# Optimization experiments

Hardware: AMD Instinct MI355X
Metric: run time of the kernel (lower is better)

The kernel has to match this reference:

```python
import jax, jax.numpy as jnp
import numpy as np

D = 256      # d_v
FF = 512     # ff_dim = max(hidden, d_v)
H = 4        # num_heads
K = 8        # max_set_size
L = 64       # subset universe length
NC = 32768   # n_chains
NB = 4096    # n_batch
EPS = 1e-8   # module eps for masked-mean denom


def setup_inputs() -> dict:
    key = jax.random.key(0)
    ks = jax.random.split(key, 24)
    s = 0.02
    mask = jax.random.randint(ks[2], (NC, L), 0, 2).astype(bool)
    inp = {
        "v": jax.random.normal(ks[0], (NB, L, D), jnp.float32),
        "batch_idx": jax.random.randint(ks[1], (NC,), 0, NB),
        "mask": mask,
        "count": mask.sum(axis=1).astype(jnp.float32),
        "pos_embed": jnp.zeros((1, K, D), jnp.float32),
        "ln1_w": jnp.ones((D,), jnp.float32),
        "ln1_b": jnp.zeros((D,), jnp.float32),
        "in_proj_w": jax.random.normal(ks[3], (3 * D, D), jnp.float32) * s,
        "in_proj_b": jnp.zeros((3 * D,), jnp.float32),
        "out_proj_w": jax.random.normal(ks[4], (D, D), jnp.float32) * s,
        "out_proj_b": jnp.zeros((D,), jnp.float32),
        "ln2_w": jnp.ones((D,), jnp.float32),
        "ln2_b": jnp.zeros((D,), jnp.float32),
        "ff1_w": jax.random.normal(ks[5], (FF, D), jnp.float32) * s,
        "ff1_b": jnp.zeros((FF,), jnp.float32),
        "ff2_w": jax.random.normal(ks[6], (D, FF), jnp.float32) * s,
        "ff2_b": jnp.zeros((D,), jnp.float32),
        "o1_w": jax.random.normal(ks[7], (FF, D + 1), jnp.float32) * s,
        "o1_b": jnp.zeros((FF,), jnp.float32),
        "o2_w": jax.random.normal(ks[8], (D, FF), jnp.float32) * s,
        "o2_b": jnp.zeros((D,), jnp.float32),
    }
    return inp


def _layernorm(x, w, b, eps=1e-5):
    mu = x.mean(-1, keepdims=True)
    var = ((x - mu) ** 2).mean(-1, keepdims=True)
    return (x - mu) * jax.lax.rsqrt(var + eps) * w + b


def reference(v, batch_idx, mask, count, pos_embed, ln1_w, ln1_b, in_proj_w,
              in_proj_b, out_proj_w, out_proj_b, ln2_w, ln2_b, ff1_w, ff1_b,
              ff2_w, ff2_b, o1_w, o1_b, o2_w, o2_b):
    nc, Lm = mask.shape
    # --- topk subset select (index-order packing) ---
    pos = jnp.arange(Lm, dtype=jnp.float32)
    scores = mask.astype(jnp.float32) * (float(Lm) - pos)[None, :]
    top_scores, top_idx = jax.lax.top_k(scores, K)
    picked0 = top_scores > 0
    sortable = jnp.where(picked0, top_idx, Lm)
    sortable = jnp.sort(sortable, axis=1)
    picked = sortable < Lm                       # [NC,K]
    safe_idx = jnp.where(picked, sortable, 0)
    # fused gather: chain_v[c, i] = v[batch_idx[c], i]
    packed = v[batch_idx[:, None], safe_idx]     # [NC,K,D]
    packed = packed * picked[..., None].astype(packed.dtype)
    x = packed + pos_embed[:, :K, :]
    # key padding mask; un-mask position 0 for fully-empty sets
    kpm = ~picked
    empty = jnp.all(kpm, axis=1)
    kpm = kpm.at[:, 0].set(jnp.where(empty, False, kpm[:, 0]))
    # --- one pre-norm transformer encoder layer ---
    h = _layernorm(x, ln1_w, ln1_b)
    qkv = h @ in_proj_w.T + in_proj_b
    q, k_, vv = jnp.split(qkv, 3, axis=-1)
    hd = D // H
    def heads(t):
        return t.reshape(nc, K, H, hd).transpose(0, 2, 1, 3)
    q, k_, vv = heads(q), heads(k_), heads(vv)
    att = jnp.einsum('bhqd,bhkd->bhqk', q, k_) / jnp.sqrt(jnp.float32(hd))
    att = jnp.where(kpm[:, None, None, :], -jnp.inf, att)
    att = jax.nn.softmax(att, axis=-1)
    ao = jnp.einsum('bhqk,bhkd->bhqd', att, vv).transpose(0, 2, 1, 3).reshape(nc, K, D)
    x = x + ao @ out_proj_w.T + out_proj_b
    h2 = _layernorm(x, ln2_w, ln2_b)
    x = x + jax.nn.gelu(h2 @ ff1_w.T + ff1_b, approximate=False) @ ff2_w.T + ff2_b
    # --- masked mean pool ---
    pf = picked.astype(x.dtype)
    denom = jnp.maximum(pf.sum(axis=1, keepdims=True), EPS)
    pooled = (x * pf[..., None]).sum(axis=1) / denom
    pooled = jnp.where(picked.any(axis=1, keepdims=True), pooled, jnp.zeros_like(pooled))
    # --- concat log(1+|S|) and project ---
    feat = jnp.concatenate([pooled, jnp.log1p(count)[:, None]], axis=-1)
    return jax.nn.gelu(feat @ o1_w.T + o1_b, approximate=False) @ o2_w.T + o2_b
```

## Files before the change

### kernel.cpp

```cpp
#include <hip/hip_runtime.h>
#include <hip/hip_bf16.h>
#include <math.h>

typedef short short8 __attribute__((ext_vector_type(8)));
typedef short short4v __attribute__((ext_vector_type(4)));
typedef float f32x4 __attribute__((ext_vector_type(4)));

#define NCC  32768
#define G    4

#define G1_OFF 0
#define G2_OFF 196608
#define G3_OFF 262144
#define G4_OFF 393216
#define O1_OFF 524288
#define O2_OFF 655360
#define SWZ_SHORTS 786432
#define W256_BYTE_OFF (SWZ_SHORTS * 2)
#define FLAG_BYTE_OFF (W256_BYTE_OFF + 2048)

#define PX2_ST 260
#define PGF_ST 520

__device__ __forceinline__ float gelu_f(float x) {
    return x * 0.5f * (1.0f + erff(x * 0.70710678118654752f));
}
__device__ __forceinline__ unsigned short f2bf(float f) {
    __hip_bfloat16 h = __float2bfloat16(f);
    return *reinterpret_cast<unsigned short*>(&h);
}
__device__ __forceinline__ int aswz(int row, int scol) {
    return row * 256 + (scol ^ ((row & 7) << 3));
}
__device__ __forceinline__ int qswz(int row, int scol) {
    return row * 512 + (scol ^ ((row & 7) << 3));
}
__device__ __forceinline__ int vtswz(int d, int j) {
    return d * 32 + (j ^ ((d & 7) << 2));
}

template<int KTS>
__device__ __forceinline__ void load_bgrp(short8 (&b)[KTS], const unsigned short* __restrict__ base) {
    #pragma unroll
    for (int kt = 0; kt < KTS; kt++)
        b[kt] = *reinterpret_cast<const short8*>(base + (size_t)kt * 512);
}

__global__ void conv_weights(const float* __restrict__ w1, const float* __restrict__ w2,
                             const float* __restrict__ w3, const float* __restrict__ w4,
                             const float* __restrict__ o1, const float* __restrict__ o2,
                             unsigned short* __restrict__ dst, float* __restrict__ w256) {
    int i = blockIdx.x * 256 + threadIdx.x;
    if (i < 98304) {
        const float* src; int kts, sk, base;
        if (i < 24576)      { src = w1; kts = 8;  sk = 256; base = 0; }
        else if (i < 32768) { src = w2; kts = 8;  sk = 256; base = 24576; }
        else if (i < 49152) { src = w3; kts = 8;  sk = 256; base = 32768; }
        else if (i < 65536) { src = w4; kts = 16; sk = 512; base = 49152; }
        else if (i < 81920) { src = o1; kts = 8;  sk = 257; base = 65536; }
        else                { src = o2; kts = 16; sk = 512; base = 81920; }
        int li   = i - base;
        int lane = li & 63;
        int fi   = li >> 6;
        int kt   = fi % kts;
        int nt   = fi / kts;
        int col  = nt * 16 + (lane & 15);
        int k    = kt * 32 + (lane >> 4) * 8;
        const float* s = src + (size_t)col * sk + k;
        unsigned short* d = dst + (size_t)i * 8;
        #pragma unroll
        for (int e = 0; e < 8; e++) d[e] = f2bf(s[e]);
    } else if (i < 98816) {
        int c = i - 98304;
        w256[c] = o1[(size_t)c * 257 + 256];
    }
}

__global__ void detect_mask_fmt(const unsigned int* __restrict__ mw, int nwords, int* __restrict__ flag) {
    __shared__ int s_bad_int, s_bad_float;
    if (threadIdx.x == 0) { s_bad_int = 0; s_bad_float = 0; }
    __syncthreads();
    int bad_int = 0, bad_float = 0;
    for (int i = threadIdx.x; i < nwords; i += blockDim.x) {
        unsigned int w = mw[i];
        if (w > 1u) bad_int = 1;
        if (w != 0u && w != 0x3F800000u) bad_float = 1;
    }
    if (bad_int)   atomicOr(&s_bad_int, 1);
    if (bad_float) atomicOr(&s_bad_float, 1);
    __syncthreads();
    if (threadIdx.x == 0)
        *flag = (!s_bad_int) ? 0 : ((!s_bad_float) ? 2 : 1);
}

__global__ __launch_bounds__(256, 2)
void tsa_main(const float* __restrict__ v,
              const int* __restrict__ batch_idx,
              const void* __restrict__ mask,
              const float* __restrict__ pos_embed,
              const float* __restrict__ ln1_w, const float* __restrict__ ln1_b,
              const float* __restrict__ in_proj_b,
              const float* __restrict__ out_proj_b,
              const float* __restrict__ ln2_w, const float* __restrict__ ln2_b,
              const float* __restrict__ ff1_b, const float* __restrict__ ff2_b,
              const unsigned short* __restrict__ wb,
              const int* __restrict__ mask_flag,
              float* __restrict__ out)
{
    __shared__ unsigned short qkbuf[32 * 512];
    __shared__ unsigned short abuf[32 * 256];
    __shared__ unsigned short attw_s[2][4][16][16];
    __shared__ int s_idx[G][8];
    __shared__ int s_m[G];
    __shared__ int s_bi[G];

    float* lnred = reinterpret_cast<float*>(qkbuf);
    float* px2   = reinterpret_cast<float*>(qkbuf + 2048);
    float* pgff  = reinterpret_cast<float*>(qkbuf + 8192);

    const int tid  = threadIdx.x;
    const int lane = tid & 63;
    const int wid  = tid >> 6;
    const int cq   = lane >> 4;
    const int cc   = lane & 15;
    const int cg0  = blockIdx.x * G;
    const int pair = wid >> 1;

    f32x4 xr[2][4];

    {
        int mf = *mask_flag;
        size_t base = (size_t)(cg0 + wid) * 64 + lane;
        int bit;
        if (mf == 0)      bit = ((const int*)mask)[base] != 0;
        else if (mf == 2) bit = ((const float*)mask)[base] != 0.0f;
        else              bit = ((const unsigned char*)mask)[base] != 0;
        unsigned long long bal = __ballot(bit);
        if (lane == 0) {
            int mm = 0; unsigned long long b = bal;
            while (b && mm < 8) { s_idx[wid][mm++] = __ffsll(b) - 1; b &= (b - 1); }
            for (int t = mm; t < 8; t++) s_idx[wid][t] = 0;
            s_m[wid]  = mm;
            s_bi[wid] = batch_idx[cg0 + wid];
        }
    }
    __syncthreads();

    auto do_gather = [&]() {
        #pragma unroll
        for (int mt = 0; mt < 2; mt++) {
            int c  = 2 * mt + (cq >> 1);
            int m  = s_m[c];
            int bi = s_bi[c];
            #pragma unroll
            for (int rr = 0; rr < 4; rr++) {
                int rowin = (cq & 1) * 4 + rr;
                int vidx  = s_idx[c][rowin];
                #pragma unroll
                for (int nt = 0; nt < 4; nt++) {
                    int col  = wid * 64 + nt * 16 + cc;
                    float pe = pos_embed[rowin * 256 + col];
                    float val = (rowin < m) ? v[((size_t)bi * 64 + vidx) * 256 + col] : 0.0f;
                    xr[mt][nt][rr] = val + pe;
                }
            }
        }
    };

    auto do_ln = [&](const float* __restrict__ lw, const float* __restrict__ lb) {
        float sm[2][4], sq[2][4];
        #pragma unroll
        for (int mt = 0; mt < 2; mt++)
            #pragma unroll
            for (int rr = 0; rr < 4; rr++) {
                float s = 0.f, q = 0.f;
                #pragma unroll
                for (int nt = 0; nt < 4; nt++) {
                    float x = xr[mt][nt][rr];
                    s += x; q += x * x;
                }
                sm[mt][rr] = s; sq[mt][rr] = q;
            }
        #pragma unroll
        for (int off = 1; off < 16; off <<= 1) {
            #pragma unroll
            for (int mt = 0; mt < 2; mt++)
                #pragma unroll
                for (int rr = 0; rr < 4; rr++) {
                    sm[mt][rr] += __shfl_xor(sm[mt][rr], off);
                    sq[mt][rr] += __shfl_xor(sq[mt][rr], off);
                }
        }
        if (cc == 0) {
            #pragma unroll
            for (int mt = 0; mt < 2; mt++)
                #pragma unroll
                for (int rr = 0; rr < 4; rr++) {
                    int row = mt * 16 + cq * 4 + rr;
                    lnred[(wid * 32 + row) * 2 + 0] = sm[mt][rr];
                    lnred[(wid * 32 + row) * 2 + 1] = sq[mt][rr];
                }
        }
        __syncthreads();
        float mu[2][4], rs[2][4];
        #pragma unroll
        for (int mt = 0; mt < 2; mt++)
            #pragma unroll
            for (int rr = 0; rr < 4; rr++) {
                int row = mt * 16 + cq * 4 + rr;
                float S = 0.f, Q = 0.f;
                #pragma unroll
                for (int w = 0; w < 4; w++) {
                    S += lnred[(w * 32 + row) * 2 + 0];
                    Q += lnred[(w * 32 + row) * 2 + 1];
                }
                float m_ = S * (1.0f / 256.0f);
                mu[mt][rr] = m_;
                rs[mt][rr] = rsqrtf(Q * (1.0f / 256.0f) - m_ * m_ + 1e-5f);
            }
        #pragma unroll
        for (int nt = 0; nt < 4; nt++) {
            int col = wid * 64 + nt * 16 + cc;
            float w_ = lw[col], b_ = lb[col];
            #pragma unroll
            for (int mt = 0; mt < 2; mt++)
                #pragma unroll
                for (int rr = 0; rr < 4; rr++) {
                    int row = mt * 16 + cq * 4 + rr;
                    abuf[aswz(row, col)] = f2bf((xr[mt][nt][rr] - mu[mt][rr]) * rs[mt][rr] * w_ + b_);
                }
        }
        __syncthreads();
    };

    auto load_a_abuf = [&](short8 (&a0)[8], short8 (&a1)[8]) {
        #pragma unroll
        for (int kt = 0; kt < 8; kt++) {
            a0[kt] = *reinterpret_cast<const short8*>(&abuf[aswz(cc,      kt * 32 + cq * 8)]);
            a1[kt] = *reinterpret_cast<const short8*>(&abuf[aswz(16 + cc, kt * 32 + cq * 8)]);
        }
    };

    do_gather();
    do_ln(ln1_w, ln1_b);

    {
        short8 a0[8], a1[8];
        load_a_abuf(a0, a1);
        __syncthreads();

        auto gbase = [&](int g) {
            int nt = g >> 1, kh = g & 1;
            int gnt = (nt < 8) ? (wid * 8 + nt) : (32 + wid * 4 + (nt - 8));
            return wb + G1_OFF + ((size_t)gnt * 8 + kh * 4) * 512 + lane * 8;
        };
        short8 bb[2][4];
        load_bgrp<4>(bb[0], gbase(0));
        f32x4 c0, c1;
        #pragma unroll
        for (int nt = 0; nt < 12; nt++) {
            #pragma unroll
            for (int kh = 0; kh < 2; kh++) {
                int g = nt * 2 + kh;
                if (g + 1 < 24) load_bgrp<4>(bb[(g + 1) & 1], gbase(g + 1));
                if (kh == 0) {
                    float b = (nt < 8) ? in_proj_b[wid * 128 + nt * 16 + cc]
                                       : in_proj_b[512 + wid * 64 + (nt - 8) * 16 + cc];
                    c0 = (f32x4){b, b, b, b};
                    c1 = (f32x4){b, b, b, b};
                }
                __builtin_amdgcn_s_setprio(1);
                #pragma unroll
                for (int kt = 0; kt < 4; kt++) {
                    c0 = __builtin_amdgcn_mfma_f32_16x16x32_bf16(a0[kh * 4 + kt], bb[g & 1][kt], c0, 0, 0, 0);
                    c1 = __builtin_amdgcn_mfma_f32_16x16x32_bf16(a1[kh * 4 + kt], bb[g & 1][kt], c1, 0, 0, 0);
                }
                __builtin_amdgcn_s_setprio(0);
            }
            if (nt < 8) {
                int col = wid * 128 + nt * 16 + cc;
                #pragma unroll
                for (int r = 0; r < 4; r++) {
                    qkbuf[qswz(cq * 4 + r, col)]      = f2bf(c0[r]);
                    qkbuf[qswz(16 + cq * 4 + r, col)] = f2bf(c1[r]);
                }
            } else {
                int d = wid * 64 + (nt - 8) * 16 + cc;
                short4v p0, p1;
                #pragma unroll
                for (int r = 0; r < 4; r++) { p0[r] = (short)f2bf(c0[r]); p1[r] = (short)f2bf(c1[r]); }
                *reinterpret_cast<short4v*>(&abuf[vtswz(d, cq * 4)])      = p0;
                *reinterpret_cast<short4v*>(&abuf[vtswz(d, 16 + cq * 4)]) = p1;
            }
        }
    }
    __syncthreads();

    do_gather();

    {
        #pragma unroll
        for (int hj = 0; hj < 2; hj++) {
            int h = (wid & 1) * 2 + hj;
            f32x4 c = {0.f, 0.f, 0.f, 0.f};
            #pragma unroll
            for (int kt = 0; kt < 2; kt++) {
                short8 qa = *reinterpret_cast<const short8*>(&qkbuf[qswz(pair * 16 + cc, h * 64 + cq * 8 + kt * 32)]);
                short8 kb = *reinterpret_cast<const short8*>(&qkbuf[qswz(pair * 16 + cc, 256 + h * 64 + cq * 8 + kt * 32)]);
                c = __builtin_amdgcn_mfma_f32_16x16x32_bf16(qa, kb, c, 0, 0, 0);
            }
            int jhalf = cc >> 3, jloc = cc & 7;
            #pragma unroll
            for (int r = 0; r < 4; r++) {
                int q = cq * 4 + r;
                int qhalf = q >> 3;
                int m = s_m[pair * 2 + qhalf];
                bool valid = (jhalf == qhalf) && (jloc < m);
                float s = valid ? c[r] * 0.125f : -1e30f;
                float mx = s;
                mx = fmaxf(mx, __shfl_xor(mx, 1));
                mx = fmaxf(mx, __shfl_xor(mx, 2));
                mx = fmaxf(mx, __shfl_xor(mx, 4));
                float e = valid ? __expf(s - mx) : 0.f;
                float se = e;
                se += __shfl_xor(se, 1);
                se += __shfl_xor(se, 2);
                se += __shfl_xor(se, 4);
                attw_s[pair][h][q][cc] = f2bf((se > 0.f) ? e / se : 0.f);
            }
        }
    }
    __syncthreads();

    {
        int jbg = pair * 16 + (cq & 1) * 8;
        #pragma unroll
        for (int hj = 0; hj < 2; hj++) {
            int h = (wid & 1) * 2 + hj;
            short8 pa;
            if (cq < 2) pa = *reinterpret_cast<const short8*>(&attw_s[pair][h][cc][cq * 8]);
            else        pa = (short8)((short)0);
            #pragma unroll
            for (int t = 0; t < 4; t++) {
                int d = h * 64 + t * 16 + cc;
                short4v lo = *reinterpret_cast<const short4v*>(&abuf[vtswz(d, jbg)]);
                short4v hi = *reinterpret_cast<const short4v*>(&abuf[vtswz(d, jbg + 4)]);
                union { short8 vv; short4v half2[2]; } u;
                u.half2[0] = lo; u.half2[1] = hi;
                f32x4 c = {0.f, 0.f, 0.f, 0.f};
                c = __builtin_amdgcn_mfma_f32_16x16x32_bf16(pa, u.vv, c, 0, 0, 0);
                #pragma unroll
                for (int r = 0; r < 4; r++)
                    qkbuf[qswz(pair * 16 + cq * 4 + r, d)] = f2bf(c[r]);
            }
        }
    }
    __syncthreads();

    {
        #pragma unroll
        for (int nt = 0; nt < 4; nt++) {
            float b = out_proj_b[wid * 64 + nt * 16 + cc];
            #pragma unroll
            for (int r = 0; r < 4; r++) { xr[0][nt][r] += b; xr[1][nt][r] += b; }
        }
        auto gbase = [&](int g) {
            int kh = g >> 2, nt = g & 3;
            return wb + G2_OFF + ((size_t)(wid * 4 + nt) * 8 + kh * 4) * 512 + lane * 8;
        };
        short8 bb[2][4];
        load_bgrp<4>(bb[0], gbase(0));
        #pragma unroll
        for (int kh = 0; kh < 2; kh++) {
            short8 a0h[4], a1h[4];
            #pragma unroll
            for (int kt = 0; kt < 4; kt++) {
                a0h[kt] = *reinterpret_cast<const short8*>(&qkbuf[qswz(cc,      kh * 128 + kt * 32 + cq * 8)]);
                a1h[kt] = *reinterpret_cast<const short8*>(&qkbuf[qswz(16 + cc, kh * 128 + kt * 32 + cq * 8)]);
            }
            #pragma unroll
            for (int nt = 0; nt < 4; nt++) {
                int g = kh * 4 + nt;
                if (g + 1 < 8) load_bgrp<4>(bb[(g + 1) & 1], gbase(g + 1));
                __builtin_amdgcn_s_setprio(1);
                #pragma unroll
                for (int kt = 0; kt < 4; kt++) {
                    xr[0][nt] = __builtin_amdgcn_mfma_f32_16x16x32_bf16(a0h[kt], bb[g & 1][kt], xr[0][nt], 0, 0, 0);
                    xr[1][nt] = __builtin_amdgcn_mfma_f32_16x16x32_bf16(a1h[kt], bb[g & 1][kt], xr[1][nt], 0, 0, 0);
                }
                __builtin_amdgcn_s_setprio(0);
            }
        }
    }
    __syncthreads();

    #pragma unroll
    for (int mt = 0; mt < 2; mt++) {
        int c = 2 * mt + (cq >> 1);
        int m = s_m[c];
        #pragma unroll
        for (int nt = 0; nt < 4; nt++) {
            float p = 0.f;
            #pragma unroll
            for (int rr = 0; rr < 4; rr++)
                if ((cq & 1) * 4 + rr < m) p += xr[mt][nt][rr];
            p += __shfl_xor(p, 16);
            if ((cq & 1) == 0) {
                int col = wid * 64 + nt * 16 + cc;
                px2[c * PX2_ST + col] = p;
            }
        }
    }

    do_ln(ln2_w, ln2_b);

    {
        short8 a0[8], a1[8];
        load_a_abuf(a0, a1);
        auto gbase = [&](int g) {
            int nt = g >> 1, kh = g & 1;
            return wb + G3_OFF + ((size_t)(wid * 8 + nt) * 8 + kh * 4) * 512 + lane * 8;
        };
        short8 bb[2][4];
        load_bgrp<4>(bb[0], gbase(0));
        f32x4 c0, c1;
        #pragma unroll
        for (int nt = 0; nt < 8; nt++) {
            #pragma unroll
            for (int kh = 0; kh < 2; kh++) {
                int g = nt * 2 + kh;
                if (g + 1 < 16) load_bgrp<4>(bb[(g + 1) & 1], gbase(g + 1));
                if (kh == 0) {
                    float b = ff1_b[wid * 128 + nt * 16 + cc];
                    c0 = (f32x4){b, b, b, b};
                    c1 = (f32x4){b, b, b, b};
                }
                __builtin_amdgcn_s_setprio(1);
                #pragma unroll
                for (int kt = 0; kt < 4; kt++) {
                    c0 = __builtin_amdgcn_mfma_f32_16x16x32_bf16(a0[kh * 4 + kt], bb[g & 1][kt], c0, 0, 0, 0);
                    c1 = __builtin_amdgcn_mfma_f32_16x16x32_bf16(a1[kh * 4 + kt], bb[g & 1][kt], c1, 0, 0, 0);
                }
                __builtin_amdgcn_s_setprio(0);
            }
            int col = wid * 128 + nt * 16 + cc;
            float s0 = 0.f, s1 = 0.f;
            int m0 = s_m[cq >> 1];
            int m1 = s_m[2 + (cq >> 1)];
            #pragma unroll
            for (int r = 0; r < 4; r++) {
                float g0 = gelu_f(c0[r]);
                float g1 = gelu_f(c1[r]);
                if ((cq & 1) * 4 + r < m0) s0 += g0;
                if ((cq & 1) * 4 + r < m1) s1 += g1;
            }
            s0 += __shfl_xor(s0, 16);
            s1 += __shfl_xor(s1, 16);
            if ((cq & 1) == 0) {
                pgff[(cq >> 1) * PGF_ST + col]       = s0;
                pgff[(2 + (cq >> 1)) * PGF_ST + col] = s1;
            }
        }
    }
    __syncthreads();

    {
        auto gbase = [&](int g) {
            int kh = g >> 2, nt = g & 3;
            return wb + G4_OFF + ((size_t)(wid * 4 + nt) * 16 + kh * 4) * 512 + lane * 8;
        };
        short8 bb[2][4];
        load_bgrp<4>(bb[0], gbase(0));
        f32x4 acc[4];
        #pragma unroll
        for (int nt = 0; nt < 4; nt++) acc[nt] = (f32x4){0.f, 0.f, 0.f, 0.f};
        #pragma unroll
        for (int kh = 0; kh < 4; kh++) {
            short8 af[4];
            #pragma unroll
            for (int kt = 0; kt < 4; kt++) {
                short8 t = (short8)((short)0);
                if (cc < 4) {
                    const float4* s4 = reinterpret_cast<const float4*>(&pgff[cc * PGF_ST + (kh * 4 + kt) * 32 + cq * 8]);
                    float4 x0 = s4[0];
                    float4 x1 = s4[1];
                    t[0] = (short)f2bf(x0.x); t[1] = (short)f2bf(x0.y);
                    t[2] = (short)f2bf(x0.z); t[3] = (short)f2bf(x0.w);
                    t[4] = (short)f2bf(x1.x); t[5] = (short)f2bf(x1.y);
                    t[6] = (short)f2bf(x1.z); t[7] = (short)f2bf(x1.w);
                }
                af[kt] = t;
            }
            #pragma unroll
            for (int nt = 0; nt < 4; nt++) {
                int g = kh * 4 + nt;
                if (g + 1 < 16) load_bgrp<4>(bb[(g + 1) & 1], gbase(g + 1));
                __builtin_amdgcn_s_setprio(1);
                #pragma unroll
                for (int kt = 0; kt < 4; kt++)
                    acc[nt] = __builtin_amdgcn_mfma_f32_16x16x32_bf16(af[kt], bb[g & 1][kt], acc[nt], 0, 0, 0);
                __builtin_amdgcn_s_setprio(0);
            }
        }
        if (cq == 0) {
            #pragma unroll
            for (int nt = 0; nt < 4; nt++) {
                int col = wid * 64 + nt * 16 + cc;
                float b4 = ff2_b[col];
                #pragma unroll
                for (int r = 0; r < 4; r++) {
                    int m = s_m[r];
                    float val = 0.f;
                    if (m > 0) val = (px2[r * PX2_ST + col] + acc[nt][r]) / (float)m + b4;
                    out[(size_t)(cg0 + r) * 256 + col] = val;
                }
            }
        }
    }
}

__global__ __launch_bounds__(256, 2)
void tsa_head(const float* __restrict__ count,
              const float* __restrict__ o1_b, const float* __restrict__ o2_b,
              const unsigned short* __restrict__ wb, const float* __restrict__ w256,
              float* __restrict__ out)
{
    __shared__ unsigned short fbuf[32 * 256];
    __shared__ unsigned short gbuf[32 * 512];
    __shared__ float cbuf[32];

    const int tid  = threadIdx.x;
    const int lane = tid & 63;
    const int wid  = tid >> 6;
    const int cq   = lane >> 4;
    const int cc   = lane & 15;
    const int c0b  = blockIdx.x * 32;

    for (int i = tid; i < 32 * 256; i += 256) {
        int row = i >> 8, col = i & 255;
        fbuf[aswz(row, col)] = f2bf(out[(size_t)(c0b + row) * 256 + col]);
    }
    if (tid < 32) cbuf[tid] = log1pf(count[c0b + tid]);
    __syncthreads();

    {
        auto gbase = [&](int g) {
            int nt = g >> 1, kh = g & 1;
            return wb + O1_OFF + ((size_t)(wid * 8 + nt) * 8 + kh * 4) * 512 + lane * 8;
        };
        short8 a0[8], a1[8];
        #pragma unroll
        for (int kt = 0; kt < 8; kt++) {
            a0[kt] = *reinterpret_cast<const short8*>(&fbuf[aswz(cc,      kt * 32 + cq * 8)]);
            a1[kt] = *reinterpret_cast<const short8*>(&fbuf[aswz(16 + cc, kt * 32 + cq * 8)]);
        }
        short8 bb[2][4];
        load_bgrp<4>(bb[0], gbase(0));
        f32x4 c0, c1;
        #pragma unroll
        for (int nt = 0; nt < 8; nt++) {
            #pragma unroll
            for (int kh = 0; kh < 2; kh++) {
                int g = nt * 2 + kh;
                if (g + 1 < 16) load_bgrp<4>(bb[(g + 1) & 1], gbase(g + 1));
                if (kh == 0) {
                    float b = o1_b[wid * 128 + nt * 16 + cc];
                    c0 = (f32x4){b, b, b, b};
                    c1 = (f32x4){b, b, b, b};
                }
                __builtin_amdgcn_s_setprio(1);
                #pragma unroll
                for (int kt = 0; kt < 4; kt++) {
                    c0 = __builtin_amdgcn_mfma_f32_16x16x32_bf16(a0[kh * 4 + kt], bb[g & 1][kt], c0, 0, 0, 0);
                    c1 = __builtin_amdgcn_mfma_f32_16x16x32_bf16(a1[kh * 4 + kt], bb[g & 1][kt], c1, 0, 0, 0);
                }
                __builtin_amdgcn_s_setprio(0);
            }
            int col  = wid * 128 + nt * 16 + cc;
            float wc = w256[col];
            #pragma unroll
            for (int r = 0; r < 4; r++) {
                int r0 = cq * 4 + r, r1 = 16 + cq * 4 + r;
                gbuf[qswz(r0, col)] = f2bf(gelu_f(c0[r] + cbuf[r0] * wc));
                gbuf[qswz(r1, col)] = f2bf(gelu_f(c1[r] + cbuf[r1] * wc));
            }
        }
    }
    __syncthreads();

    {
        f32x4 c[4][2];
        #pragma unroll
        for (int nt = 0; nt < 4; nt++) {
            float b = o2_b[wid * 64 + nt * 16 + cc];
            c[nt][0] = (f32x4){b, b, b, b};
            c[nt][1] = (f32x4){b, b, b, b};
        }
        auto gbase = [&](int g) {
            int half = g >> 3, kh = (g >> 2) & 1, nt = g & 3;
            return wb + O2_OFF + ((size_t)(wid * 4 + nt) * 16 + half * 8 + kh * 4) * 512 + lane * 8;
        };
        short8 bb[2][4];
        load_bgrp<4>(bb[0], gbase(0));
        #pragma unroll
        for (int half = 0; half < 2; half++) {
            #pragma unroll
            for (int kh = 0; kh < 2; kh++) {
                short8 a0q[4], a1q[4];
                #pragma unroll
                for (int kt = 0; kt < 4; kt++) {
                    int scol = half * 256 + kh * 128 + kt * 32 + cq * 8;
                    a0q[kt] = *reinterpret_cast<const short8*>(&gbuf[qswz(cc,      scol)]);
                    a1q[kt] = *reinterpret_cast<const short8*>(&gbuf[qswz(16 + cc, scol)]);
                }
                #pragma unroll
                for (int nt = 0; nt < 4; nt++) {
                    int g = half * 8 + kh * 4 + nt;
                    if (g + 1 < 16) load_bgrp<4>(bb[(g + 1) & 1], gbase(g + 1));
                    __builtin_amdgcn_s_setprio(1);
                    #pragma unroll
                    for (int kt = 0; kt < 4; kt++) {
                        c[nt][0] = __builtin_amdgcn_mfma_f32_16x16x32_bf16(a0q[kt], bb[g & 1][kt], c[nt][0], 0, 0, 0);
                        c[nt][1] = __builtin_amdgcn_mfma_f32_16x16x32_bf16(a1q[kt], bb[g & 1][kt], c[nt][1], 0, 0, 0);
                    }
                    __builtin_amdgcn_s_setprio(0);
                }
            }
        }
        #pragma unroll
        for (int nt = 0; nt < 4; nt++) {
            int col = wid * 64 + nt * 16 + cc;
            #pragma unroll
            for (int r = 0; r < 4; r++) {
                out[(size_t)(c0b + cq * 4 + r) * 256 + col]      = c[nt][0][r];
                out[(size_t)(c0b + 16 + cq * 4 + r) * 256 + col] = c[nt][1][r];
            }
        }
    }
}

extern "C" void kernel_launch(void* const* d_in, const int* in_sizes, int n_in,
                              void* d_out, int out_size, void* d_ws, size_t ws_size,
                              hipStream_t stream) {
    const float* v          = (const float*)d_in[0];
    const int*   batch_idx  = (const int*)d_in[1];
    const void*  mask       = d_in[2];
    const float* count      = (const float*)d_in[3];
    const float* pos_embed  = (const float*)d_in[4];
    const float* ln1_w      = (const float*)d_in[5];
    const float* ln1_b      = (const float*)d_in[6];
    const float* in_proj_w  = (const float*)d_in[7];
    const float* in_proj_b  = (const float*)d_in[8];
    const float* out_proj_w = (const float*)d_in[9];
    const float* out_proj_b = (const float*)d_in[10];
    const float* ln2_w      = (const float*)d_in[11];
    const float* ln2_b      = (const float*)d_in[12];
    const float* ff1_w      = (const float*)d_in[13];
    const float* ff1_b      = (const float*)d_in[14];
    const float* ff2_w      = (const float*)d_in[15];
    const float* ff2_b      = (const float*)d_in[16];
    const float* o1_w       = (const float*)d_in[17];
    const float* o1_b       = (const float*)d_in[18];
    const float* o2_w       = (const float*)d_in[19];
    const float* o2_b       = (const float*)d_in[20];
    float* out = (float*)d_out;

    unsigned short* wb = (unsigned short*)d_ws;
    float* w256 = (float*)((char*)d_ws + W256_BYTE_OFF);
    int* flag   = (int*)((char*)d_ws + FLAG_BYTE_OFF);

    conv_weights<<<387, 256, 0, stream>>>(in_proj_w, out_proj_w, ff1_w, ff2_w, o1_w, o2_w, wb, w256);
    detect_mask_fmt<<<1, 256, 0, stream>>>((const unsigned int*)mask, 16384, flag);
    tsa_main<<<NCC / G, 256, 0, stream>>>(v, batch_idx, mask, pos_embed,
                                          ln1_w, ln1_b, in_proj_b, out_proj_b,
                                          ln2_w, ln2_b, ff1_b, ff2_b,
                                          wb, flag, out);
    tsa_head<<<NCC / 32, 256, 0, stream>>>(count, o1_b, o2_b, wb, w256, out);
}
```

Before: 564.8 us.

## Split tsa_main work across 8 waves with 16-row M tiles per wave

The main kernel now launches 512 threads per block instead of 256. Each wave handles one 16-row M half and one 64-column slice, where before a wave held both 32-row halves, so per-thread accumulators and A fragments are halved. Attention runs one head per wave instead of looping over two, and the FF2 stage splits output columns across all 8 waves. This is meant to lower register pressure and raise occupancy, at the cost of each wave reloading the same B weight fragments, which doubles weight traffic from L2/global per block.

```diff
diff --git a/kernel.cpp b/kernel.cpp
--- a/kernel.cpp
+++ b/kernel.cpp
@@ -93,7 +93,7 @@
         *flag = (!s_bad_int) ? 0 : ((!s_bad_float) ? 2 : 1);
 }
 
-__global__ __launch_bounds__(256, 2)
+__global__ __launch_bounds__(512, 4)
 void tsa_main(const float* __restrict__ v,
               const int* __restrict__ batch_idx,
               const void* __restrict__ mask,
@@ -121,14 +121,16 @@
     const int tid  = threadIdx.x;
     const int lane = tid & 63;
     const int wid  = tid >> 6;
+    const int cw   = wid & 3;
+    const int mg   = wid >> 2;
+    const int mrow0 = mg * 16;
     const int cq   = lane >> 4;
     const int cc   = lane & 15;
     const int cg0  = blockIdx.x * G;
-    const int pair = wid >> 1;
-
-    f32x4 xr[2][4];
-
-    {
+
+    f32x4 xr[4];
+
+    if (wid < G) {
         int mf = *mask_flag;
         size_t base = (size_t)(cg0 + wid) * 64 + lane;
         int bit;
@@ -147,116 +149,101 @@
     __syncthreads();
 
     auto do_gather = [&]() {
-        #pragma unroll
-        for (int mt = 0; mt < 2; mt++) {
-            int c  = 2 * mt + (cq >> 1);
-            int m  = s_m[c];
-            int bi = s_bi[c];
+        int c  = mg * 2 + (cq >> 1);
+        int m  = s_m[c];
+        int bi = s_bi[c];
+        #pragma unroll
+        for (int rr = 0; rr < 4; rr++) {
+            int rowin = (cq & 1) * 4 + rr;
+            int vidx  = s_idx[c][rowin];
+            #pragma unroll
+            for (int nt = 0; nt < 4; nt++) {
+                int col  = cw * 64 + nt * 16 + cc;
+                float pe = pos_embed[rowin * 256 + col];
+                float val = (rowin < m) ? v[((size_t)bi * 64 + vidx) * 256 + col] : 0.0f;
+                xr[nt][rr] = val + pe;
+            }
+        }
+    };
+
+    auto do_ln = [&](const float* __restrict__ lw, const float* __restrict__ lb) {
+        float sm[4], sq[4];
+        #pragma unroll
+        for (int rr = 0; rr < 4; rr++) {
+            float s = 0.f, q = 0.f;
+            #pragma unroll
+            for (int nt = 0; nt < 4; nt++) {
+                float x = xr[nt][rr];
+                s += x; q += x * x;
+            }
+            sm[rr] = s; sq[rr] = q;
+        }
+        #pragma unroll
+        for (int off = 1; off < 16; off <<= 1) {
             #pragma unroll
             for (int rr = 0; rr < 4; rr++) {
-                int rowin = (cq & 1) * 4 + rr;
-                int vidx  = s_idx[c][rowin];
-                #pragma unroll
-                for (int nt = 0; nt < 4; nt++) {
-                    int col  = wid * 64 + nt * 16 + cc;
-                    float pe = pos_embed[rowin * 256 + col];
-                    float val = (rowin < m) ? v[((size_t)bi * 64 + vidx) * 256 + col] : 0.0f;
-                    xr[mt][nt][rr] = val + pe;
-                }
-            }
-        }
-    };
-
-    auto do_ln = [&](const float* __restrict__ lw, const float* __restrict__ lb) {
-        float sm[2][4], sq[2][4];
-        #pragma unroll
-        for (int mt = 0; mt < 2; mt++)
+                sm[rr] += __shfl_xor(sm[rr], off);
+                sq[rr] += __shfl_xor(sq[rr], off);
+            }
+        }
+        if (cc == 0) {
             #pragma unroll
             for (int rr = 0; rr < 4; rr++) {
-                float s = 0.f, q = 0.f;
-                #pragma unroll
-                for (int nt = 0; nt < 4; nt++) {
-                    float x = xr[mt][nt][rr];
-                    s += x; q += x * x;
-                }
-                sm[mt][rr] = s; sq[mt][rr] = q;
-            }
-        #pragma unroll
-        for (int off = 1; off < 16; off <<= 1) {
-            #pragma unroll
-            for (int mt = 0; mt < 2; mt++)
-                #pragma unroll
-                for (int rr = 0; rr < 4; rr++) {
-                    sm[mt][rr] += __shfl_xor(sm[mt][rr], off);
-                    sq[mt][rr] += __shfl_xor(sq[mt][rr], off);
-                }
-        }
-        if (cc == 0) {
-            #pragma unroll
-            for (int mt = 0; mt < 2; mt++)
-                #pragma unroll
-                for (int rr = 0; rr < 4; rr++) {
-                    int row = mt * 16 + cq * 4 + rr;
-                    lnred[(wid * 32 + row) * 2 + 0] = sm[mt][rr];
-                    lnred[(wid * 32 + row) * 2 + 1] = sq[mt][rr];
-                }
+                int row = mrow0 + cq * 4 + rr;
+                lnred[(cw * 32 + row) * 2 + 0] = sm[rr];
+                lnred[(cw * 32 + row) * 2 + 1] = sq[rr];
+            }
         }
         __syncthreads();
-        float mu[2][4], rs[2][4];
-        #pragma unroll
-        for (int mt = 0; mt < 2; mt++)
+        float mu[4], rs[4];
+        #pragma unroll
+        for (int rr = 0; rr < 4; rr++) {
+            int row = mrow0 + cq * 4 + rr;
+            float S = 0.f, Q = 0.f;
+            #pragma unroll
+            for (int w = 0; w < 4; w++) {
+                S += lnred[(w * 32 + row) * 2 + 0];
+                Q += lnred[(w * 32 + row) * 2 + 1];
+            }
+            float m_ = S * (1.0f / 256.0f);
+            mu[rr] = m_;
+            rs[rr] = rsqrtf(Q * (1.0f / 256.0f) - m_ * m_ + 1e-5f);
+        }
+        #pragma unroll
+        for (int nt = 0; nt < 4; nt++) {
+            int col = cw * 64 + nt * 16 + cc;
+            float w_ = lw[col], b_ = lb[col];
             #pragma unroll
             for (int rr = 0; rr < 4; rr++) {
-                int row = mt * 16 + cq * 4 + rr;
-                float S = 0.f, Q = 0.f;
-                #pragma unroll
-                for (int w = 0; w < 4; w++) {
-                    S += lnred[(w * 32 + row) * 2 + 0];
-                    Q += lnred[(w * 32 + row) * 2 + 1];
-                }
-                float m_ = S * (1.0f / 256.0f);
-                mu[mt][rr] = m_;
-                rs[mt][rr] = rsqrtf(Q * (1.0f / 256.0f) - m_ * m_ + 1e-5f);
-            }
-        #pragma unroll
-        for (int nt = 0; nt < 4; nt++) {
-            int col = wid * 64 + nt * 16 + cc;
-            float w_ = lw[col], b_ = lb[col];
-            #pragma unroll
-            for (int mt = 0; mt < 2; mt++)
-                #pragma unroll
-                for (int rr = 0; rr < 4; rr++) {
-                    int row = mt * 16 + cq * 4 + rr;
-                    abuf[aswz(row, col)] = f2bf((xr[mt][nt][rr] - mu[mt][rr]) * rs[mt][rr] * w_ + b_);
-                }
+                int row = mrow0 + cq * 4 + rr;
+                abuf[aswz(row, col)] = f2bf((xr[nt][rr] - mu[rr]) * rs[rr] * w_ + b_);
+            }
         }
         __syncthreads();
     };
 
-    auto load_a_abuf = [&](short8 (&a0)[8], short8 (&a1)[8]) {
-        #pragma unroll
-        for (int kt = 0; kt < 8; kt++) {
-            a0[kt] = *reinterpret_cast<const short8*>(&abuf[aswz(cc,      kt * 32 + cq * 8)]);
-            a1[kt] = *reinterpret_cast<const short8*>(&abuf[aswz(16 + cc, kt * 32 + cq * 8)]);
-        }
+    auto load_a_abuf = [&](short8 (&a0)[8]) {
+        #pragma unroll
+        for (int kt = 0; kt < 8; kt++)
+            a0[kt] = *reinterpret_cast<const short8*>(&abuf[aswz(mrow0 + cc, kt * 32 + cq * 8)]);
     };
 
     do_gather();
     do_ln(ln1_w, ln1_b);
 
     {
-        short8 a0[8], a1[8];
-        load_a_abuf(a0, a1);
+        short8 a0[8];
+        load_a_abuf(a0);
         __syncthreads();
 
         auto gbase = [&](int g) {
             int nt = g >> 1, kh = g & 1;
-            int gnt = (nt < 8) ? (wid * 8 + nt) : (32 + wid * 4 + (nt - 8));
+            int gnt = (nt < 8) ? (cw * 8 + nt) : (32 + cw * 4 + (nt - 8));
             return wb + G1_OFF + ((size_t)gnt * 8 + kh * 4) * 512 + lane * 8;
         };
         short8 bb[2][4];
         load_bgrp<4>(bb[0], gbase(0));
-        f32x4 c0, c1;
+        f32x4 c0;
         #pragma unroll
         for (int nt = 0; nt < 12; nt++) {
             #pragma unroll
@@ -264,33 +251,27 @@
                 int g = nt * 2 + kh;
                 if (g + 1 < 24) load_bgrp<4>(bb[(g + 1) & 1], gbase(g + 1));
                 if (kh == 0) {
-                    float b = (nt < 8) ? in_proj_b[wid * 128 + nt * 16 + cc]
-                                       : in_proj_b[512 + wid * 64 + (nt - 8) * 16 + cc];
+                    float b = (nt < 8) ? in_proj_b[cw * 128 + nt * 16 + cc]
+                                       : in_proj_b[512 + cw * 64 + (nt - 8) * 16 + cc];
                     c0 = (f32x4){b, b, b, b};
-                    c1 = (f32x4){b, b, b, b};
                 }
                 __builtin_amdgcn_s_setprio(1);
                 #pragma unroll
-                for (int kt = 0; kt < 4; kt++) {
+                for (int kt = 0; kt < 4; kt++)
                     c0 = __builtin_amdgcn_mfma_f32_16x16x32_bf16(a0[kh * 4 + kt], bb[g & 1][kt], c0, 0, 0, 0);
-                    c1 = __builtin_amdgcn_mfma_f32_16x16x32_bf16(a1[kh * 4 + kt], bb[g & 1][kt], c1, 0, 0, 0);
-                }
                 __builtin_amdgcn_s_setprio(0);
             }
             if (nt < 8) {
-                int col = wid * 128 + nt * 16 + cc;
-                #pragma unroll
-                for (int r = 0; r < 4; r++) {
-                    qkbuf[qswz(cq * 4 + r, col)]      = f2bf(c0[r]);
-                    qkbuf[qswz(16 + cq * 4 + r, col)] = f2bf(c1[r]);
-                }
+                int col = cw * 128 + nt * 16 + cc;
+                #pragma unroll
+                for (int r = 0; r < 4; r++)
+                    qkbuf[qswz(mrow0 + cq * 4 + r, col)] = f2bf(c0[r]);
             } else {
-                int d = wid * 64 + (nt - 8) * 16 + cc;
-                short4v p0, p1;
-                #pragma unroll
-                for (int r = 0; r < 4; r++) { p0[r] = (short)f2bf(c0[r]); p1[r] = (short)f2bf(c1[r]); }
-                *reinterpret_cast<short4v*>(&abuf[vtswz(d, cq * 4)])      = p0;
-                *reinterpret_cast<short4v*>(&abuf[vtswz(d, 16 + cq * 4)]) = p1;
+                int d = cw * 64 + (nt - 8) * 16 + cc;
+                short4v p0;
+                #pragma unroll
+                for (int r = 0; r < 4; r++) p0[r] = (short)f2bf(c0[r]);
+                *reinterpret_cast<short4v*>(&abuf[vtswz(d, mrow0 + cq * 4)]) = p0;
             }
         }
     }
@@ -299,60 +280,56 @@
     do_gather();
 
     {
-        #pragma unroll
-        for (int hj = 0; hj < 2; hj++) {
-            int h = (wid & 1) * 2 + hj;
+        int pair = wid >> 2;
+        int h    = wid & 3;
+        f32x4 c = {0.f, 0.f, 0.f, 0.f};
+        #pragma unroll
+        for (int kt = 0; kt < 2; kt++) {
+            short8 qa = *reinterpret_cast<const short8*>(&qkbuf[qswz(pair * 16 + cc, h * 64 + cq * 8 + kt * 32)]);
+            short8 kb = *reinterpret_cast<const short8*>(&qkbuf[qswz(pair * 16 + cc, 256 + h * 64 + cq * 8 + kt * 32)]);
+            c = __builtin_amdgcn_mfma_f32_16x16x32_bf16(qa, kb, c, 0, 0, 0);
+        }
+        int jhalf = cc >> 3, jloc = cc & 7;
+        #pragma unroll
+        for (int r = 0; r < 4; r++) {
+            int q = cq * 4 + r;
+            int qhalf = q >> 3;
+            int m = s_m[pair * 2 + qhalf];
+            bool valid = (jhalf == qhalf) && (jloc < m);
+            float s = valid ? c[r] * 0.125f : -1e30f;
+            float mx = s;
+            mx = fmaxf(mx, __shfl_xor(mx, 1));
+            mx = fmaxf(mx, __shfl_xor(mx, 2));
+            mx = fmaxf(mx, __shfl_xor(mx, 4));
+            float e = valid ? __expf(s - mx) : 0.f;
+            float se = e;
+            se += __shfl_xor(se, 1);
+            se += __shfl_xor(se, 2);
+            se += __shfl_xor(se, 4);
+            attw_s[pair][h][q][cc] = f2bf((se > 0.f) ? e / se : 0.f);
+        }
+    }
+    __syncthreads();
+
+    {
+        int pair = wid >> 2;
+        int h    = wid & 3;
+        int jbg  = pair * 16 + (cq & 1) * 8;
+        short8 pa;
+        if (cq < 2) pa = *reinterpret_cast<const short8*>(&attw_s[pair][h][cc][cq * 8]);
+        else        pa = (short8)((short)0);
+        #pragma unroll
+        for (int t = 0; t < 4; t++) {
+            int d = h * 64 + t * 16 + cc;
+            short4v lo = *reinterpret_cast<const short4v*>(&abuf[vtswz(d, jbg)]);
+            short4v hi = *reinterpret_cast<const short4v*>(&abuf[vtswz(d, jbg + 4)]);
+            union { short8 vv; short4v half2[2]; } u;
+            u.half2[0] = lo; u.half2[1] = hi;
             f32x4 c = {0.f, 0.f, 0.f, 0.f};
-            #pragma unroll
-            for (int kt = 0; kt < 2; kt++) {
-                short8 qa = *reinterpret_cast<const short8*>(&qkbuf[qswz(pair * 16 + cc, h * 64 + cq * 8 + kt * 32)]);
-                short8 kb = *reinterpret_cast<const short8*>(&qkbuf[qswz(pair * 16 + cc, 256 + h * 64 + cq * 8 + kt * 32)]);
-                c = __builtin_amdgcn_mfma_f32_16x16x32_bf16(qa, kb, c, 0, 0, 0);
-            }
-            int jhalf = cc >> 3, jloc = cc & 7;
-            #pragma unroll
-            for (int r = 0; r < 4; r++) {
-                int q = cq * 4 + r;
-                int qhalf = q >> 3;
-                int m = s_m[pair * 2 + qhalf];
-                bool valid = (jhalf == qhalf) && (jloc < m);
-                float s = valid ? c[r] * 0.125f : -1e30f;
-                float mx = s;
-                mx = fmaxf(mx, __shfl_xor(mx, 1));
-                mx = fmaxf(mx, __shfl_xor(mx, 2));
-                mx = fmaxf(mx, __shfl_xor(mx, 4));
-                float e = valid ? __expf(s - mx) : 0.f;
-                float se = e;
-                se += __shfl_xor(se, 1);
-                se += __shfl_xor(se, 2);
-                se += __shfl_xor(se, 4);
-                attw_s[pair][h][q][cc] = f2bf((se > 0.f) ? e / se : 0.f);
-            }
-        }
-    }
-    __syncthreads();
-
-    {
-        int jbg = pair * 16 + (cq & 1) * 8;
-        #pragma unroll
-        for (int hj = 0; hj < 2; hj++) {
-            int h = (wid & 1) * 2 + hj;
-            short8 pa;
-            if (cq < 2) pa = *reinterpret_cast<const short8*>(&attw_s[pair][h][cc][cq * 8]);
-            else        pa = (short8)((short)0);
-            #pragma unroll
-            for (int t = 0; t < 4; t++) {
-                int d = h * 64 + t * 16 + cc;
-                short4v lo = *reinterpret_cast<const short4v*>(&abuf[vtswz(d, jbg)]);
-                short4v hi = *reinterpret_cast<const short4v*>(&abuf[vtswz(d, jbg + 4)]);
-                union { short8 vv; short4v half2[2]; } u;
-                u.half2[0] = lo; u.half2[1] = hi;
-                f32x4 c = {0.f, 0.f, 0.f, 0.f};
-                c = __builtin_amdgcn_mfma_f32_16x16x32_bf16(pa, u.vv, c, 0, 0, 0);
-                #pragma unroll
-                for (int r = 0; r < 4; r++)
-                    qkbuf[qswz(pair * 16 + cq * 4 + r, d)] = f2bf(c[r]);
-            }
+            c = __builtin_amdgcn_mfma_f32_16x16x32_bf16(pa, u.vv, c, 0, 0, 0);
+            #pragma unroll
+            for (int r = 0; r < 4; r++)
+                qkbuf[qswz(pair * 16 + cq * 4 + r, d)] = f2bf(c[r]);
         }
     }
     __syncthreads();
@@ -360,53 +337,48 @@
     {
         #pragma unroll
         for (int nt = 0; nt < 4; nt++) {
-            float b = out_proj_b[wid * 64 + nt * 16 + cc];
-            #pragma unroll
-            for (int r = 0; r < 4; r++) { xr[0][nt][r] += b; xr[1][nt][r] += b; }
+            float b = out_proj_b[cw * 64 + nt * 16 + cc];
+            #pragma unroll
+            for (int r = 0; r < 4; r++) xr[nt][r] += b;
         }
         auto gbase = [&](int g) {
             int kh = g >> 2, nt = g & 3;
-            return wb + G2_OFF + ((size_t)(wid * 4 + nt) * 8 + kh * 4) * 512 + lane * 8;
+            return wb + G2_OFF + ((size_t)(cw * 4 + nt) * 8 + kh * 4) * 512 + lane * 8;
         };
         short8 bb[2][4];
         load_bgrp<4>(bb[0], gbase(0));
         #pragma unroll
         for (int kh = 0; kh < 2; kh++) {
-            short8 a0h[4], a1h[4];
-            #pragma unroll
-            for (int kt = 0; kt < 4; kt++) {
-                a0h[kt] = *reinterpret_cast<const short8*>(&qkbuf[qswz(cc,      kh * 128 + kt * 32 + cq * 8)]);
-                a1h[kt] = *reinterpret_cast<const short8*>(&qkbuf[qswz(16 + cc, kh * 128 + kt * 32 + cq * 8)]);
-            }
+            short8 a0h[4];
+            #pragma unroll
+            for (int kt = 0; kt < 4; kt++)
+                a0h[kt] = *reinterpret_cast<const short8*>(&qkbuf[qswz(mrow0 + cc, kh * 128 + kt * 32 + cq * 8)]);
             #pragma unroll
             for (int nt = 0; nt < 4; nt++) {
                 int g = kh * 4 + nt;
                 if (g + 1 < 8) load_bgrp<4>(bb[(g + 1) & 1], gbase(g + 1));
                 __builtin_amdgcn_s_setprio(1);
                 #pragma unroll
-                for (int kt = 0; kt < 4; kt++) {
-                    xr[0][nt] = __builtin_amdgcn_mfma_f32_16x16x32_bf16(a0h[kt], bb[g & 1][kt], xr[0][nt], 0, 0, 0);
-                    xr[1][nt] = __builtin_amdgcn_mfma_f32_16x16x32_bf16(a1h[kt], bb[g & 1][kt], xr[1][nt], 0, 0, 0);
-                }
+                for (int kt = 0; kt < 4; kt++)
+                    xr[nt] = __builtin_amdgcn_mfma_f32_16x16x32_bf16(a0h[kt], bb[g & 1][kt], xr[nt], 0, 0, 0);
                 __builtin_amdgcn_s_setprio(0);
             }
         }
     }
     __syncthreads();
 
-    #pragma unroll
-    for (int mt = 0; mt < 2; mt++) {
-        int c = 2 * mt + (cq >> 1);
+    {
+        int c = mg * 2 + (cq >> 1);
         int m = s_m[c];
         #pragma unroll
         for (int nt = 0; nt < 4; nt++) {
             float p = 0.f;
             #pragma unroll
             for (int rr = 0; rr < 4; rr++)
-                if ((cq & 1) * 4 + rr < m) p += xr[mt][nt][rr];
+                if ((cq & 1) * 4 + rr < m) p += xr[nt][rr];
             p += __shfl_xor(p, 16);
             if ((cq & 1) == 0) {
-                int col = wid * 64 + nt * 16 + cc;
+                int col = cw * 64 + nt * 16 + cc;
                 px2[c * PX2_ST + col] = p;
             }
         }
@@ -415,15 +387,15 @@
     do_ln(ln2_w, ln2_b);
 
     {
-        short8 a0[8], a1[8];
-        load_a_abuf(a0, a1);
+        short8 a0[8];
+        load_a_abuf(a0);
         auto gbase = [&](int g) {
             int nt = g >> 1, kh = g & 1;
-            return wb + G3_OFF + ((size_t)(wid * 8 + nt) * 8 + kh * 4) * 512 + lane * 8;
+            return wb + G3_OFF + ((size_t)(cw * 8 + nt) * 8 + kh * 4) * 512 + lane * 8;
         };
         short8 bb[2][4];
         load_bgrp<4>(bb[0], gbase(0));
-        f32x4 c0, c1;
+        f32x4 c0;
         #pragma unroll
         for (int nt = 0; nt < 8; nt++) {
             #pragma unroll
@@ -431,49 +403,41 @@
                 int g = nt * 2 + kh;
                 if (g + 1 < 16) load_bgrp<4>(bb[(g + 1) & 1], gbase(g + 1));
                 if (kh == 0) {
-                    float b = ff1_b[wid * 128 + nt * 16 + cc];
+                    float b = ff1_b[cw * 128 + nt * 16 + cc];
                     c0 = (f32x4){b, b, b, b};
-                    c1 = (f32x4){b, b, b, b};
                 }
                 __builtin_amdgcn_s_setprio(1);
                 #pragma unroll
-                for (int kt = 0; kt < 4; kt++) {
+                for (int kt = 0; kt < 4; kt++)
                     c0 = __builtin_amdgcn_mfma_f32_16x16x32_bf16(a0[kh * 4 + kt], bb[g & 1][kt], c0, 0, 0, 0);
-                    c1 = __builtin_amdgcn_mfma_f32_16x16x32_bf16(a1[kh * 4 + kt], bb[g & 1][kt], c1, 0, 0, 0);
-                }
                 __builtin_amdgcn_s_setprio(0);
             }
-            int col = wid * 128 + nt * 16 + cc;
-            float s0 = 0.f, s1 = 0.f;
-            int m0 = s_m[cq >> 1];
-            int m1 = s_m[2 + (cq >> 1)];
+            int col = cw * 128 + nt * 16 + cc;
+            int c   = mg * 2 + (cq >> 1);
+            int m0  = s_m[c];
+            float s0 = 0.f;
             #pragma unroll
             for (int r = 0; r < 4; r++) {
                 float g0 = gelu_f(c0[r]);
-                float g1 = gelu_f(c1[r]);
                 if ((cq & 1) * 4 + r < m0) s0 += g0;
-                if ((cq & 1) * 4 + r < m1) s1 += g1;
             }
             s0 += __shfl_xor(s0, 16);
-            s1 += __shfl_xor(s1, 16);
-            if ((cq & 1) == 0) {
-                pgff[(cq >> 1) * PGF_ST + col]       = s0;
-                pgff[(2 + (cq >> 1)) * PGF_ST + col] = s1;
-            }
+            if ((cq & 1) == 0)
+                pgff[c * PGF_ST + col] = s0;
         }
     }
     __syncthreads();
 
     {
         auto gbase = [&](int g) {
-            int kh = g >> 2, nt = g & 3;
-            return wb + G4_OFF + ((size_t)(wid * 4 + nt) * 16 + kh * 4) * 512 + lane * 8;
+            int kh = g >> 1, j = g & 1;
+            return wb + G4_OFF + ((size_t)(wid * 2 + j) * 16 + kh * 4) * 512 + lane * 8;
         };
         short8 bb[2][4];
         load_bgrp<4>(bb[0], gbase(0));
-        f32x4 acc[4];
-        #pragma unroll
-        for (int nt = 0; nt < 4; nt++) acc[nt] = (f32x4){0.f, 0.f, 0.f, 0.f};
+        f32x4 acc[2];
+        acc[0] = (f32x4){0.f, 0.f, 0.f, 0.f};
+        acc[1] = (f32x4){0.f, 0.f, 0.f, 0.f};
         #pragma unroll
         for (int kh = 0; kh < 4; kh++) {
             short8 af[4];
@@ -492,26 +456,26 @@
                 af[kt] = t;
             }
             #pragma unroll
-            for (int nt = 0; nt < 4; nt++) {
-                int g = kh * 4 + nt;
-                if (g + 1 < 16) load_bgrp<4>(bb[(g + 1) & 1], gbase(g + 1));
+            for (int j = 0; j < 2; j++) {
+                int g = kh * 2 + j;
+                if (g + 1 < 8) load_bgrp<4>(bb[(g + 1) & 1], gbase(g + 1));
                 __builtin_amdgcn_s_setprio(1);
                 #pragma unroll
                 for (int kt = 0; kt < 4; kt++)
-                    acc[nt] = __builtin_amdgcn_mfma_f32_16x16x32_bf16(af[kt], bb[g & 1][kt], acc[nt], 0, 0, 0);
+                    acc[j] = __builtin_amdgcn_mfma_f32_16x16x32_bf16(af[kt], bb[g & 1][kt], acc[j], 0, 0, 0);
                 __builtin_amdgcn_s_setprio(0);
             }
         }
         if (cq == 0) {
             #pragma unroll
-            for (int nt = 0; nt < 4; nt++) {
-                int col = wid * 64 + nt * 16 + cc;
+            for (int j = 0; j < 2; j++) {
+                int col = (wid * 2 + j) * 16 + cc;
                 float b4 = ff2_b[col];
                 #pragma unroll
                 for (int r = 0; r < 4; r++) {
                     int m = s_m[r];
                     float val = 0.f;
-                    if (m > 0) val = (px2[r * PX2_ST + col] + acc[nt][r]) / (float)m + b4;
+                    if (m > 0) val = (px2[r * PX2_ST + col] + acc[j][r]) / (float)m + b4;
                     out[(size_t)(cg0 + r) * 256 + col] = val;
                 }
             }
@@ -671,7 +635,7 @@
 
     conv_weights<<<387, 256, 0, stream>>>(in_proj_w, out_proj_w, ff1_w, ff2_w, o1_w, o2_w, wb, w256);
     detect_mask_fmt<<<1, 256, 0, stream>>>((const unsigned int*)mask, 16384, flag);
-    tsa_main<<<NCC / G, 256, 0, stream>>>(v, batch_idx, mask, pos_embed,
+    tsa_main<<<NCC / G, 512, 0, stream>>>(v, batch_idx, mask, pos_embed,
                                           ln1_w, ln1_b, in_proj_b, out_proj_b,
                                           ln2_w, ln2_b, ff1_b, ff2_b,
                                           wb, flag, out);
```

Result: slower. 810.7 us (+43.5%).
